# Kernel optimization log

Measured on AMD Instinct MI355X. Metric: run time of the kernel, lower is better.

Reference implementation:

```python
import jax, jax.numpy as jnp
import numpy as np

N, M, B = 1024, 8192, 8192  # W: [N, M], x: [B, N]
BLOCK = 32


def activation_quant(x):
    # per-tensor symmetric int8 fake-quant with STE
    scale = 127.0 / jnp.clip(jnp.max(jnp.abs(x)), 1e-8, None)
    x_q = jnp.clip(jnp.round(x * scale), -128.0, 127.0) / scale
    return x + jax.lax.stop_gradient(x_q - x)


def weight_quant_q2_k(w, block_size=BLOCK):
    # blockwise 2-bit quant with top-2 outliers kept at 4-bit, STE
    shape = w.shape
    wf = w.reshape(-1)
    n = wf.shape[0]
    pad = (-n) % block_size
    wf = jnp.pad(wf, (0, pad))
    blocks = wf.reshape(-1, block_size)
    scales = jnp.clip(jnp.max(jnp.abs(blocks), axis=1, keepdims=True), 1e-8, None)
    nb = blocks / scales
    k = min(2, block_size)
    _, top_idx = jax.lax.top_k(jnp.abs(nb), k)
    rows = jnp.arange(nb.shape[0])[:, None]
    top_mask = jnp.zeros(nb.shape, dtype=bool).at[rows, top_idx].set(True)
    q4 = jnp.round(nb * 7.0) / 7.0
    abs_nb = jnp.abs(nb)
    q2 = jnp.sign(nb) * jnp.where(abs_nb > 0.66, 1.0, 1.0 / 3.0)
    q = jnp.where(top_mask, q4, q2) * scales
    w_q = q.reshape(-1)[:n].reshape(shape)
    return w + jax.lax.stop_gradient(w_q - w)


def setup_inputs() -> dict:
    key = jax.random.key(0)
    k1, k2, k3 = jax.random.split(key, 3)
    x = jax.random.normal(k1, (B, N), dtype=jnp.float32)
    W = jax.random.normal(k2, (N, M), dtype=jnp.float32) / np.float32(np.sqrt(M))
    b = jax.random.normal(k3, (N,), dtype=jnp.float32)
    idx = jnp.arange(M // 2, dtype=jnp.int32)            # expanded (quantized) columns
    idx_comp = jnp.arange(M // 2, M, dtype=jnp.int32)    # continuous columns
    return {"x": x, "W": W, "b": b, "idx": idx, "idx_comp": idx_comp}


def reference(x, W, b, idx, idx_comp):
    W_exp_q = weight_quant_q2_k(jnp.take(W, idx, axis=1))   # [N, M/2]
    W_cont = jnp.take(W, idx_comp, axis=1)                  # [N, M/2]
    hidden_exp = activation_quant(x) @ W_exp_q              # [B, M/2]
    hidden_cont = x @ W_cont                                # [B, M/2]
    hidden = (jnp.zeros((x.shape[0], M), dtype=x.dtype)
              .at[:, idx].set(hidden_exp)
              .at[:, idx_comp].set(hidden_cont))            # scatter back to [B, M]
    h_exp = activation_quant(hidden[:, idx])
    out = jax.nn.relu(h_exp @ W_exp_q.T + hidden[:, idx_comp] @ W_cont.T + b)
    return out
```

## Files before the change

### kernel.cpp

```cpp
#include <hip/hip_runtime.h>
#include <hip/hip_bf16.h>
#include <cstdint>


using bf16x8 = __attribute__((ext_vector_type(8))) __bf16;
using f32x4  = __attribute__((ext_vector_type(4))) float;

typedef const __attribute__((address_space(1))) void g_void;
typedef __attribute__((address_space(3))) void l_void;

__device__ __forceinline__ void gload16(const void* g, void* l) {
  __builtin_amdgcn_global_load_lds((g_void*)g, (l_void*)l, 16, 0, 0);
}

__device__ __forceinline__ ushort f2bf(float f) {
  union { float f; unsigned u; } c; c.f = f;
  unsigned r = c.u + 0x7FFFu + ((c.u >> 16) & 1u);
  return (ushort)(r >> 16);
}
__device__ __forceinline__ float bf2f(ushort u) {
  union { unsigned u; float f; } c; c.u = ((unsigned)u) << 16;
  return c.f;
}

__global__ void prep_wa_kernel(const float* __restrict__ W,
                               const float4* __restrict__ x,
                               ushort* __restrict__ Wq,
                               ushort* __restrict__ WqT,
                               ushort* __restrict__ Wcb,
                               unsigned* __restrict__ amax_bits) {
  const int bidx = blockIdx.x;
  const int tid = threadIdx.x;

  if (bidx < 1024) {
    __shared__ __align__(16) ushort tile[64][72];
    const int rt = bidx >> 6;
    const int ct = bidx & 63;
    const int r0 = rt * 64, c0 = ct * 64;
    const int e = tid & 31;
    const int hw = tid >> 5;
    #pragma unroll
    for (int it = 0; it < 16; ++it) {
      const int g = it * 8 + hw;
      const int row = g >> 1;
      const int cg = (g & 1) * 32;
      const float w = W[(size_t)(r0 + row) * 8192 + c0 + cg + e];
      float aw = fabsf(w);
      float m = aw;
      #pragma unroll
      for (int d = 1; d <= 16; d <<= 1) m = fmaxf(m, __shfl_xor(m, d));
      int idx = (aw == m) ? e : 32;
      #pragma unroll
      for (int d = 1; d <= 16; d <<= 1) idx = min(idx, __shfl_xor(idx, d));
      const int i1 = idx;
      float a2 = (e == i1) ? -1.f : aw;
      float m2 = a2;
      #pragma unroll
      for (int d = 1; d <= 16; d <<= 1) m2 = fmaxf(m2, __shfl_xor(m2, d));
      int idx2 = (a2 == m2) ? e : 32;
      #pragma unroll
      for (int d = 1; d <= 16; d <<= 1) idx2 = min(idx2, __shfl_xor(idx2, d));
      const int i2 = idx2;

      const float scale = fmaxf(m, 1e-8f);
      const float nb = w / scale;
      float q;
      if (e == i1 || e == i2) {
        q = rintf(nb * 7.f) / 7.f;
      } else {
        float s = (nb > 0.f) ? 1.f : ((nb < 0.f) ? -1.f : 0.f);
        q = s * ((fabsf(nb) > 0.66f) ? 1.f : (1.f / 3.f));
      }
      const ushort qb = f2bf(q * scale);
      Wq[(size_t)(r0 + row) * 4096 + c0 + cg + e] = qb;
      tile[cg + e][row] = qb;
    }
    __syncthreads();
    const int c = tid >> 2;
    const int q4 = (tid & 3) * 16;
    uint4 v0 = *(const uint4*)&tile[c][q4];
    uint4 v1 = *(const uint4*)&tile[c][q4 + 8];
    *(uint4*)(WqT + (size_t)(c0 + c) * 1024 + r0 + q4) = v0;
    *(uint4*)(WqT + (size_t)(c0 + c) * 1024 + r0 + q4 + 8) = v1;
  } else if (bidx < 5120) {
    const int u = (bidx - 1024) * 256 + tid;
    const int row = u >> 10;
    const int c4 = u & 1023;
    float4 v = *(const float4*)(W + (size_t)row * 8192 + 4096 + c4 * 4);
    ushort4 o;
    o.x = f2bf(v.x); o.y = f2bf(v.y); o.z = f2bf(v.z); o.w = f2bf(v.w);
    *(ushort4*)(Wcb + (size_t)row * 4096 + c4 * 4) = o;
  } else {
    float m = 0.f;
    const int base = (bidx - 5120) * 256 + tid;
    const int stride = 2048 * 256;
    for (int i = base; i < 8192 * 1024 / 4; i += stride) {
      float4 v = x[i];
      m = fmaxf(m, fmaxf(fmaxf(fabsf(v.x), fabsf(v.y)),
                         fmaxf(fabsf(v.z), fabsf(v.w))));
    }
    #pragma unroll
    for (int off = 32; off > 0; off >>= 1) m = fmaxf(m, __shfl_down(m, off));
    __shared__ float wm[4];
    int lane = tid & 63, wave = tid >> 6;
    if (lane == 0) wm[wave] = m;
    __syncthreads();
    if (tid == 0) {
      float r = fmaxf(fmaxf(wm[0], wm[1]), fmaxf(wm[2], wm[3]));
      atomicMax(amax_bits, __float_as_uint(r));
    }
  }
}

__global__ void prep_x_kernel(const float4* __restrict__ x,
                              const unsigned* __restrict__ amax_bits,
                              uint4* __restrict__ xq, uint4* __restrict__ xbf) {
  const float amax = fmaxf(__uint_as_float(*amax_bits), 1e-8f);
  const float scale = 127.f / amax;
  const int base = blockIdx.x * 256 + threadIdx.x;
  const int stride = 2048 * 256;
  const int n8 = 8192 * 1024 / 8;
  for (int i = base; i < n8; i += stride) {
    float4 a = x[i * 2], b = x[i * 2 + 1];
    float v[8] = {a.x, a.y, a.z, a.w, b.x, b.y, b.z, b.w};
    unsigned qw[4], bw[4];
    #pragma unroll
    for (int j = 0; j < 4; ++j) {
      float q0 = fminf(fmaxf(rintf(v[2 * j] * scale), -128.f), 127.f) / scale;
      float q1 = fminf(fmaxf(rintf(v[2 * j + 1] * scale), -128.f), 127.f) / scale;
      qw[j] = (unsigned)f2bf(q0) | ((unsigned)f2bf(q1) << 16);
      bw[j] = (unsigned)f2bf(v[2 * j]) | ((unsigned)f2bf(v[2 * j + 1]) << 16);
    }
    xq[i] = make_uint4(qw[0], qw[1], qw[2], qw[3]);
    xbf[i] = make_uint4(bw[0], bw[1], bw[2], bw[3]);
  }
}

__global__ __launch_bounds__(256, 2) void gemm1_kernel(
    const ushort* __restrict__ Wcb,
    ushort* __restrict__ G,
    const ushort* __restrict__ Aq, const ushort* __restrict__ BT,
    ushort* __restrict__ Hexp, unsigned* __restrict__ amax_bits) {
  __shared__ __align__(16) ushort As[2][128 * 32];
  __shared__ __align__(16) ushort Bs[2][128 * 32];
  __shared__ float wredmax[4];

  const int bidx = blockIdx.x;
  const int tid = threadIdx.x;
  const int lane = tid & 63, wave = tid >> 6;
  const int l15 = lane & 15, quad = lane >> 4;
  const int wm = (wave >> 1) << 6, wn = (wave & 1) << 6;
  const int sel = (quad ^ ((l15 >> 1) & 3)) * 8;
  const int scs = ((tid & 3) ^ ((tid >> 3) & 3)) * 8;

  ushort* Asl0 = As[0] + tid * 8; ushort* Asl1 = As[1] + tid * 8;
  ushort* Bsl0 = Bs[0] + tid * 8; ushort* Bsl1 = Bs[1] + tid * 8;

  f32x4 acc[4][4];
  #pragma unroll
  for (int i = 0; i < 4; ++i)
    #pragma unroll
    for (int j = 0; j < 4; ++j) acc[i][j] = (f32x4){0.f, 0.f, 0.f, 0.f};

  if (bidx < 64) {
    const int gy = bidx >> 3, gx = bidx & 7;
    const int i0 = gy * 128, j0 = gx * 128;
    const ushort* Ag = Wcb + (size_t)(i0 + (tid >> 2)) * 4096 + scs;
    const ushort* Bg = Wcb + (size_t)(j0 + (tid >> 2)) * 4096 + scs;
    for (int k0 = 0; k0 < 4096; k0 += 64) {
      __syncthreads();
      gload16(Ag + k0, Asl0);
      gload16(Ag + (size_t)64 * 4096 + k0, Asl0 + 64 * 32);
      gload16(Bg + k0, Bsl0);
      gload16(Bg + (size_t)64 * 4096 + k0, Bsl0 + 64 * 32);
      gload16(Ag + k0 + 32, Asl1);
      gload16(Ag + (size_t)64 * 4096 + k0 + 32, Asl1 + 64 * 32);
      gload16(Bg + k0 + 32, Bsl1);
      gload16(Bg + (size_t)64 * 4096 + k0 + 32, Bsl1 + 64 * 32);
      __syncthreads();
      #pragma unroll
      for (int p = 0; p < 2; ++p) {
        bf16x8 af[4], bfr[4];
        #pragma unroll
        for (int i = 0; i < 4; ++i)
          af[i] = *(const bf16x8*)&As[p][(wm + i * 16 + l15) * 32 + sel];
        #pragma unroll
        for (int j = 0; j < 4; ++j)
          bfr[j] = *(const bf16x8*)&Bs[p][(wn + j * 16 + l15) * 32 + sel];
        #pragma unroll
        for (int i = 0; i < 4; ++i)
          #pragma unroll
          for (int j = 0; j < 4; ++j)
            acc[i][j] = __builtin_amdgcn_mfma_f32_16x16x32_bf16(af[i], bfr[j], acc[i][j], 0, 0, 0);
      }
    }
    const int row0 = i0 + wm + quad * 4;
    const int col0 = j0 + wn + l15;
    #pragma unroll
    for (int i = 0; i < 4; ++i)
      #pragma unroll
      for (int j = 0; j < 4; ++j)
        #pragma unroll
        for (int r = 0; r < 4; ++r)
          G[(size_t)(row0 + i * 16 + r) * 1024 + (col0 + j * 16)] = f2bf(acc[i][j][r]);
    return;
  }

  const int l = bidx - 64;
  const int xcd = l & 7;
  const int s = l >> 3;
  const int t = (xcd << 2) | (s >> 6);
  const int u = s & 63;
  const int bx = ((t & 3) << 3) | (u & 7);
  const int by = ((t >> 2) << 3) | (u >> 3);

  const ushort* Ag = Aq + (size_t)(by * 128 + (tid >> 2)) * 1024 + scs;
  const ushort* Bg = BT + (size_t)(bx * 128 + (tid >> 2)) * 1024 + scs;

  for (int k0 = 0; k0 < 1024; k0 += 64) {
    __syncthreads();
    gload16(Ag + k0, Asl0);
    gload16(Ag + 64 * 1024 + k0, Asl0 + 64 * 32);
    gload16(Bg + k0, Bsl0);
    gload16(Bg + 64 * 1024 + k0, Bsl0 + 64 * 32);
    gload16(Ag + k0 + 32, Asl1);
    gload16(Ag + 64 * 1024 + k0 + 32, Asl1 + 64 * 32);
    gload16(Bg + k0 + 32, Bsl1);
    gload16(Bg + 64 * 1024 + k0 + 32, Bsl1 + 64 * 32);
    __syncthreads();

    #pragma unroll
    for (int p = 0; p < 2; ++p) {
      bf16x8 af[4], bfr[4];
      #pragma unroll
      for (int i = 0; i < 4; ++i)
        af[i] = *(const bf16x8*)&As[p][(wm + i * 16 + l15) * 32 + sel];
      #pragma unroll
      for (int j = 0; j < 4; ++j)
        bfr[j] = *(const bf16x8*)&Bs[p][(wn + j * 16 + l15) * 32 + sel];
      #pragma unroll
      for (int i = 0; i < 4; ++i)
        #pragma unroll
        for (int j = 0; j < 4; ++j)
          acc[i][j] = __builtin_amdgcn_mfma_f32_16x16x32_bf16(af[i], bfr[j], acc[i][j], 0, 0, 0);
    }
  }

  const int row0 = by * 128 + wm + quad * 4;
  const int col0 = bx * 128 + wn + l15;
  float lmax = 0.f;
  #pragma unroll
  for (int i = 0; i < 4; ++i)
    #pragma unroll
    for (int j = 0; j < 4; ++j)
      #pragma unroll
      for (int r = 0; r < 4; ++r) {
        float v = acc[i][j][r];
        lmax = fmaxf(lmax, fabsf(v));
        Hexp[(size_t)(row0 + i * 16 + r) * 4096 + (col0 + j * 16)] = f2bf(v);
      }

  #pragma unroll
  for (int off = 32; off > 0; off >>= 1)
    lmax = fmaxf(lmax, __shfl_down(lmax, off));
  if (lane == 0) wredmax[wave] = lmax;
  __syncthreads();
  if (tid == 0) {
    float m = fmaxf(fmaxf(wredmax[0], wredmax[1]), fmaxf(wredmax[2], wredmax[3]));
    atomicMax(amax_bits, __float_as_uint(m));
  }
}

__global__ void quant_h_kernel(ushort* __restrict__ H,
                               const unsigned* __restrict__ amax_bits) {
  const float amax = fmaxf(__uint_as_float(*amax_bits), 1e-8f);
  const float scale = 127.f / amax;
  const int n8 = 8192 * 4096 / 8;
  for (int i = blockIdx.x * blockDim.x + threadIdx.x; i < n8;
       i += gridDim.x * blockDim.x) {
    uint4* p = (uint4*)H + i;
    uint4 a = *p;
    unsigned w[4] = {a.x, a.y, a.z, a.w};
    #pragma unroll
    for (int j = 0; j < 4; ++j) {
      float lo = bf2f((ushort)(w[j] & 0xFFFF));
      float hi = bf2f((ushort)(w[j] >> 16));
      lo = fminf(fmaxf(rintf(lo * scale), -128.f), 127.f) / scale;
      hi = fminf(fmaxf(rintf(hi * scale), -128.f), 127.f) / scale;
      w[j] = (unsigned)f2bf(lo) | ((unsigned)f2bf(hi) << 16);
    }
    *p = make_uint4(w[0], w[1], w[2], w[3]);
  }
}

__global__ __launch_bounds__(256, 2) void gemm2_kernel(
    const ushort* __restrict__ Hq, const ushort* __restrict__ Wq,
    const ushort* __restrict__ Xb, const ushort* __restrict__ G,
    const float* __restrict__ bias, float* __restrict__ out) {
  __shared__ __align__(16) ushort As[2][128 * 32];
  __shared__ __align__(16) ushort Bs[2][128 * 32];

  const int l = blockIdx.x;
  const int xcd = l & 7;
  const int s = l >> 3;
  const int by = (xcd << 3) | (s >> 3);
  const int bx = s & 7;

  const int tid = threadIdx.x;
  const int lane = tid & 63, wave = tid >> 6;
  const int wm = (wave >> 1) << 6, wn = (wave & 1) << 6;
  const int l15 = lane & 15, quad = lane >> 4;
  const int sel = (quad ^ ((l15 >> 1) & 3)) * 8;
  const int scs = ((tid & 3) ^ ((tid >> 3) & 3)) * 8;

  ushort* Asl0 = As[0] + tid * 8; ushort* Asl1 = As[1] + tid * 8;
  ushort* Bsl0 = Bs[0] + tid * 8; ushort* Bsl1 = Bs[1] + tid * 8;

  f32x4 acc[4][4];
  #pragma unroll
  for (int i = 0; i < 4; ++i)
    #pragma unroll
    for (int j = 0; j < 4; ++j) acc[i][j] = (f32x4){0.f, 0.f, 0.f, 0.f};

  {
    const ushort* Ag = Hq + (size_t)(by * 128 + (tid >> 2)) * 4096 + scs;
    const ushort* Bg = Wq + (size_t)(bx * 128 + (tid >> 2)) * 4096 + scs;
    for (int k0 = 0; k0 < 4096; k0 += 64) {
      __syncthreads();
      gload16(Ag + k0, Asl0);
      gload16(Ag + (size_t)64 * 4096 + k0, Asl0 + 64 * 32);
      gload16(Bg + k0, Bsl0);
      gload16(Bg + (size_t)64 * 4096 + k0, Bsl0 + 64 * 32);
      gload16(Ag + k0 + 32, Asl1);
      gload16(Ag + (size_t)64 * 4096 + k0 + 32, Asl1 + 64 * 32);
      gload16(Bg + k0 + 32, Bsl1);
      gload16(Bg + (size_t)64 * 4096 + k0 + 32, Bsl1 + 64 * 32);
      __syncthreads();
      #pragma unroll
      for (int p = 0; p < 2; ++p) {
        bf16x8 af[4], bfr[4];
        #pragma unroll
        for (int i = 0; i < 4; ++i)
          af[i] = *(const bf16x8*)&As[p][(wm + i * 16 + l15) * 32 + sel];
        #pragma unroll
        for (int j = 0; j < 4; ++j)
          bfr[j] = *(const bf16x8*)&Bs[p][(wn + j * 16 + l15) * 32 + sel];
        #pragma unroll
        for (int i = 0; i < 4; ++i)
          #pragma unroll
          for (int j = 0; j < 4; ++j)
            acc[i][j] = __builtin_amdgcn_mfma_f32_16x16x32_bf16(af[i], bfr[j], acc[i][j], 0, 0, 0);
      }
    }
  }
  {
    const ushort* Ag = Xb + (size_t)(by * 128 + (tid >> 2)) * 1024 + scs;
    const ushort* Bg = G + (size_t)(bx * 128 + (tid >> 2)) * 1024 + scs;
    for (int k0 = 0; k0 < 1024; k0 += 64) {
      __syncthreads();
      gload16(Ag + k0, Asl0);
      gload16(Ag + 64 * 1024 + k0, Asl0 + 64 * 32);
      gload16(Bg + k0, Bsl0);
      gload16(Bg + 64 * 1024 + k0, Bsl0 + 64 * 32);
      gload16(Ag + k0 + 32, Asl1);
      gload16(Ag + 64 * 1024 + k0 + 32, Asl1 + 64 * 32);
      gload16(Bg + k0 + 32, Bsl1);
      gload16(Bg + 64 * 1024 + k0 + 32, Bsl1 + 64 * 32);
      __syncthreads();
      #pragma unroll
      for (int p = 0; p < 2; ++p) {
        bf16x8 af[4], bfr[4];
        #pragma unroll
        for (int i = 0; i < 4; ++i)
          af[i] = *(const bf16x8*)&As[p][(wm + i * 16 + l15) * 32 + sel];
        #pragma unroll
        for (int j = 0; j < 4; ++j)
          bfr[j] = *(const bf16x8*)&Bs[p][(wn + j * 16 + l15) * 32 + sel];
        #pragma unroll
        for (int i = 0; i < 4; ++i)
          #pragma unroll
          for (int j = 0; j < 4; ++j)
            acc[i][j] = __builtin_amdgcn_mfma_f32_16x16x32_bf16(af[i], bfr[j], acc[i][j], 0, 0, 0);
      }
    }
  }

  const int row0 = by * 128 + wm + quad * 4;
  const int col0 = bx * 128 + wn + l15;
  #pragma unroll
  for (int i = 0; i < 4; ++i)
    #pragma unroll
    for (int j = 0; j < 4; ++j) {
      float bv = bias[col0 + j * 16];
      #pragma unroll
      for (int r = 0; r < 4; ++r) {
        float v = acc[i][j][r] + bv;
        v = fmaxf(v, 0.f);
        out[(size_t)(row0 + i * 16 + r) * 1024 + (col0 + j * 16)] = v;
      }
    }
}

extern "C" void kernel_launch(void* const* d_in, const int* in_sizes, int n_in,
                              void* d_out, int out_size, void* d_ws, size_t ws_size,
                              hipStream_t stream) {
  (void)in_sizes; (void)n_in; (void)out_size; (void)ws_size;
  const float* x = (const float*)d_in[0];
  const float* W = (const float*)d_in[1];
  const float* b = (const float*)d_in[2];

  char* ws = (char*)d_ws;
  unsigned* scal = (unsigned*)ws;
  ushort* xq   = (ushort*)(ws + 256);
  ushort* xbf  = xq   + (size_t)8192 * 1024;
  ushort* Wq   = xbf  + (size_t)8192 * 1024;
  ushort* WqT  = Wq   + (size_t)1024 * 4096;
  ushort* Wcb  = WqT  + (size_t)4096 * 1024;
  ushort* G    = Wcb  + (size_t)1024 * 4096;
  ushort* Hexp = G    + (size_t)1024 * 1024;

  hipMemsetAsync(scal, 0, 256, stream);
  prep_wa_kernel<<<7168, 256, 0, stream>>>(W, (const float4*)x, Wq, WqT, Wcb, scal);
  prep_x_kernel<<<2048, 256, 0, stream>>>((const float4*)x, scal,
                                          (uint4*)xq, (uint4*)xbf);
  gemm1_kernel<<<2112, 256, 0, stream>>>(Wcb, G, xq, WqT, Hexp, scal + 1);
  quant_h_kernel<<<4096, 256, 0, stream>>>(Hexp, scal + 1);
  gemm2_kernel<<<512, 256, 0, stream>>>(Hexp, Wq, xbf, G, b, (float*)d_out);
}
```

Measured before the change: 341.5 us.

## Fuse prep and quant stages into persistent kernels with grid barriers

Merges prep_wa and prep_x into one persistent 512-block kernel that uses a software grid barrier after the x amax reduction. gemm1 and the H quantisation are merged the same way: each block handles several output tiles, joins a grid barrier on the global amax, then re-quantises its own tiles while they are likely still in cache. This removes two kernel launches and one full standalone pass over H. In exchange it relies on all 512 blocks being co-resident to avoid deadlock, and the persistent grid may load-balance the tiles less evenly.

```diff
diff --git a/kernel.cpp b/kernel.cpp
--- a/kernel.cpp
+++ b/kernel.cpp
@@ -23,22 +23,74 @@
   return c.f;
 }
 
-__global__ void prep_wa_kernel(const float* __restrict__ W,
-                               const float4* __restrict__ x,
-                               ushort* __restrict__ Wq,
-                               ushort* __restrict__ WqT,
-                               ushort* __restrict__ Wcb,
-                               unsigned* __restrict__ amax_bits) {
-  const int bidx = blockIdx.x;
+__device__ __forceinline__ void gridbar(unsigned* cnt) {
+  __syncthreads();
+  if (threadIdx.x == 0) {
+    __threadfence();
+    __hip_atomic_fetch_add(cnt, 1u, __ATOMIC_ACQ_REL, __HIP_MEMORY_SCOPE_AGENT);
+    while (__hip_atomic_load(cnt, __ATOMIC_ACQUIRE, __HIP_MEMORY_SCOPE_AGENT) <
+           512u)
+      __builtin_amdgcn_s_sleep(2);
+  }
+  __syncthreads();
+}
+
+template <int STRIDE>
+__device__ __forceinline__ void kloop(const ushort* Ag, const ushort* Bg,
+                                      int kbeg, int kend, ushort* As, ushort* Bs,
+                                      f32x4 (&acc)[4][4], int wm, int wn,
+                                      int l15, int quad, int sel) {
   const int tid = threadIdx.x;
-
-  if (bidx < 1024) {
-    __shared__ __align__(16) ushort tile[64][72];
-    const int rt = bidx >> 6;
-    const int ct = bidx & 63;
+  ushort* Asl0 = As + tid * 8;        ushort* Asl1 = As + 4096 + tid * 8;
+  ushort* Bsl0 = Bs + tid * 8;        ushort* Bsl1 = Bs + 4096 + tid * 8;
+  for (int k0 = kbeg; k0 < kend; k0 += 64) {
+    __syncthreads();
+    gload16(Ag + k0, Asl0);
+    gload16(Ag + (size_t)64 * STRIDE + k0, Asl0 + 64 * 32);
+    gload16(Bg + k0, Bsl0);
+    gload16(Bg + (size_t)64 * STRIDE + k0, Bsl0 + 64 * 32);
+    gload16(Ag + k0 + 32, Asl1);
+    gload16(Ag + (size_t)64 * STRIDE + k0 + 32, Asl1 + 64 * 32);
+    gload16(Bg + k0 + 32, Bsl1);
+    gload16(Bg + (size_t)64 * STRIDE + k0 + 32, Bsl1 + 64 * 32);
+    __syncthreads();
+    #pragma unroll
+    for (int p = 0; p < 2; ++p) {
+      bf16x8 af[4], bfr[4];
+      #pragma unroll
+      for (int i = 0; i < 4; ++i)
+        af[i] = *(const bf16x8*)&As[p * 4096 + (wm + i * 16 + l15) * 32 + sel];
+      #pragma unroll
+      for (int j = 0; j < 4; ++j)
+        bfr[j] = *(const bf16x8*)&Bs[p * 4096 + (wn + j * 16 + l15) * 32 + sel];
+      #pragma unroll
+      for (int i = 0; i < 4; ++i)
+        #pragma unroll
+        for (int j = 0; j < 4; ++j)
+          acc[i][j] = __builtin_amdgcn_mfma_f32_16x16x32_bf16(af[i], bfr[j],
+                                                              acc[i][j], 0, 0, 0);
+    }
+  }
+}
+
+__global__ __launch_bounds__(256, 2) void prep_kernel(
+    const float* __restrict__ W, const float4* __restrict__ x,
+    ushort* __restrict__ Wq, ushort* __restrict__ WqT,
+    ushort* __restrict__ Wcb, unsigned* __restrict__ bar,
+    unsigned* __restrict__ amaxx,
+    uint4* __restrict__ xq, uint4* __restrict__ xbf) {
+  __shared__ __align__(16) ushort tile[64][72];
+  __shared__ float sred[4];
+  const int b = blockIdx.x;
+  const int tid = threadIdx.x;
+  const int lane = tid & 63, wave = tid >> 6;
+
+  #pragma unroll 1
+  for (int tt = 0; tt < 2; ++tt) {
+    const int t = b * 2 + tt;
+    const int rt = t >> 6, ct = t & 63;
     const int r0 = rt * 64, c0 = ct * 64;
-    const int e = tid & 31;
-    const int hw = tid >> 5;
+    const int e = tid & 31, hw = tid >> 5;
     #pragma unroll
     for (int it = 0; it < 16; ++it) {
       const int g = it * 8 + hw;
@@ -82,47 +134,44 @@
     uint4 v1 = *(const uint4*)&tile[c][q4 + 8];
     *(uint4*)(WqT + (size_t)(c0 + c) * 1024 + r0 + q4) = v0;
     *(uint4*)(WqT + (size_t)(c0 + c) * 1024 + r0 + q4 + 8) = v1;
-  } else if (bidx < 5120) {
-    const int u = (bidx - 1024) * 256 + tid;
+    __syncthreads();
+  }
+
+  for (int u = b * 256 + tid; u < 1024 * 1024; u += 512 * 256) {
     const int row = u >> 10;
     const int c4 = u & 1023;
     float4 v = *(const float4*)(W + (size_t)row * 8192 + 4096 + c4 * 4);
     ushort4 o;
     o.x = f2bf(v.x); o.y = f2bf(v.y); o.z = f2bf(v.z); o.w = f2bf(v.w);
     *(ushort4*)(Wcb + (size_t)row * 4096 + c4 * 4) = o;
-  } else {
+  }
+
+  {
     float m = 0.f;
-    const int base = (bidx - 5120) * 256 + tid;
-    const int stride = 2048 * 256;
-    for (int i = base; i < 8192 * 1024 / 4; i += stride) {
+    for (int i = b * 256 + tid; i < 8192 * 1024 / 4; i += 512 * 256) {
       float4 v = x[i];
       m = fmaxf(m, fmaxf(fmaxf(fabsf(v.x), fabsf(v.y)),
                          fmaxf(fabsf(v.z), fabsf(v.w))));
     }
     #pragma unroll
     for (int off = 32; off > 0; off >>= 1) m = fmaxf(m, __shfl_down(m, off));
-    __shared__ float wm[4];
-    int lane = tid & 63, wave = tid >> 6;
-    if (lane == 0) wm[wave] = m;
+    if (lane == 0) sred[wave] = m;
     __syncthreads();
     if (tid == 0) {
-      float r = fmaxf(fmaxf(wm[0], wm[1]), fmaxf(wm[2], wm[3]));
-      atomicMax(amax_bits, __float_as_uint(r));
-    }
-  }
-}
-
-__global__ void prep_x_kernel(const float4* __restrict__ x,
-                              const unsigned* __restrict__ amax_bits,
-                              uint4* __restrict__ xq, uint4* __restrict__ xbf) {
-  const float amax = fmaxf(__uint_as_float(*amax_bits), 1e-8f);
+      float r = fmaxf(fmaxf(sred[0], sred[1]), fmaxf(sred[2], sred[3]));
+      atomicMax(amaxx, __float_as_uint(r));
+    }
+  }
+  gridbar(&bar[0]);
+
+  const float amax = fmaxf(
+      __uint_as_float(__hip_atomic_load(amaxx, __ATOMIC_ACQUIRE,
+                                        __HIP_MEMORY_SCOPE_AGENT)),
+      1e-8f);
   const float scale = 127.f / amax;
-  const int base = blockIdx.x * 256 + threadIdx.x;
-  const int stride = 2048 * 256;
-  const int n8 = 8192 * 1024 / 8;
-  for (int i = base; i < n8; i += stride) {
-    float4 a = x[i * 2], b = x[i * 2 + 1];
-    float v[8] = {a.x, a.y, a.z, a.w, b.x, b.y, b.z, b.w};
+  for (int i = b * 256 + tid; i < 8192 * 1024 / 8; i += 512 * 256) {
+    float4 a = x[i * 2], v2 = x[i * 2 + 1];
+    float v[8] = {a.x, a.y, a.z, a.w, v2.x, v2.y, v2.z, v2.w};
     unsigned qw[4], bw[4];
     #pragma unroll
     for (int j = 0; j < 4; ++j) {
@@ -137,15 +186,14 @@
 }
 
 __global__ __launch_bounds__(256, 2) void gemm1_kernel(
-    const ushort* __restrict__ Wcb,
-    ushort* __restrict__ G,
+    const ushort* __restrict__ Wcb, ushort* __restrict__ G,
     const ushort* __restrict__ Aq, const ushort* __restrict__ BT,
-    ushort* __restrict__ Hexp, unsigned* __restrict__ amax_bits) {
-  __shared__ __align__(16) ushort As[2][128 * 32];
-  __shared__ __align__(16) ushort Bs[2][128 * 32];
-  __shared__ float wredmax[4];
-
-  const int bidx = blockIdx.x;
+    ushort* __restrict__ Hexp, unsigned* __restrict__ bar,
+    unsigned* __restrict__ amaxh) {
+  __shared__ __align__(16) ushort As[8192];
+  __shared__ __align__(16) ushort Bs[8192];
+  __shared__ float sred[4];
+  const int b = blockIdx.x;
   const int tid = threadIdx.x;
   const int lane = tid & 63, wave = tid >> 6;
   const int l15 = lane & 15, quad = lane >> 4;
@@ -153,47 +201,17 @@
   const int sel = (quad ^ ((l15 >> 1) & 3)) * 8;
   const int scs = ((tid & 3) ^ ((tid >> 3) & 3)) * 8;
 
-  ushort* Asl0 = As[0] + tid * 8; ushort* Asl1 = As[1] + tid * 8;
-  ushort* Bsl0 = Bs[0] + tid * 8; ushort* Bsl1 = Bs[1] + tid * 8;
-
-  f32x4 acc[4][4];
-  #pragma unroll
-  for (int i = 0; i < 4; ++i)
-    #pragma unroll
-    for (int j = 0; j < 4; ++j) acc[i][j] = (f32x4){0.f, 0.f, 0.f, 0.f};
-
-  if (bidx < 64) {
-    const int gy = bidx >> 3, gx = bidx & 7;
+  if (b < 64) {
+    const int gy = b >> 3, gx = b & 7;
     const int i0 = gy * 128, j0 = gx * 128;
+    f32x4 acc[4][4];
+    #pragma unroll
+    for (int i = 0; i < 4; ++i)
+      #pragma unroll
+      for (int j = 0; j < 4; ++j) acc[i][j] = (f32x4){0.f, 0.f, 0.f, 0.f};
     const ushort* Ag = Wcb + (size_t)(i0 + (tid >> 2)) * 4096 + scs;
     const ushort* Bg = Wcb + (size_t)(j0 + (tid >> 2)) * 4096 + scs;
-    for (int k0 = 0; k0 < 4096; k0 += 64) {
-      __syncthreads();
-      gload16(Ag + k0, Asl0);
-      gload16(Ag + (size_t)64 * 4096 + k0, Asl0 + 64 * 32);
-      gload16(Bg + k0, Bsl0);
-      gload16(Bg + (size_t)64 * 4096 + k0, Bsl0 + 64 * 32);
-      gload16(Ag + k0 + 32, Asl1);
-      gload16(Ag + (size_t)64 * 4096 + k0 + 32, Asl1 + 64 * 32);
-      gload16(Bg + k0 + 32, Bsl1);
-      gload16(Bg + (size_t)64 * 4096 + k0 + 32, Bsl1 + 64 * 32);
-      __syncthreads();
-      #pragma unroll
-      for (int p = 0; p < 2; ++p) {
-        bf16x8 af[4], bfr[4];
-        #pragma unroll
-        for (int i = 0; i < 4; ++i)
-          af[i] = *(const bf16x8*)&As[p][(wm + i * 16 + l15) * 32 + sel];
-        #pragma unroll
-        for (int j = 0; j < 4; ++j)
-          bfr[j] = *(const bf16x8*)&Bs[p][(wn + j * 16 + l15) * 32 + sel];
-        #pragma unroll
-        for (int i = 0; i < 4; ++i)
-          #pragma unroll
-          for (int j = 0; j < 4; ++j)
-            acc[i][j] = __builtin_amdgcn_mfma_f32_16x16x32_bf16(af[i], bfr[j], acc[i][j], 0, 0, 0);
-      }
-    }
+    kloop<4096>(Ag, Bg, 0, 4096, As, Bs, acc, wm, wn, l15, quad, sel);
     const int row0 = i0 + wm + quad * 4;
     const int col0 = j0 + wn + l15;
     #pragma unroll
@@ -202,94 +220,86 @@
       for (int j = 0; j < 4; ++j)
         #pragma unroll
         for (int r = 0; r < 4; ++r)
-          G[(size_t)(row0 + i * 16 + r) * 1024 + (col0 + j * 16)] = f2bf(acc[i][j][r]);
+          G[(size_t)(row0 + i * 16 + r) * 1024 + (col0 + j * 16)] =
+              f2bf(acc[i][j][r]);
+    gridbar(&bar[1]);
     return;
   }
 
-  const int l = bidx - 64;
-  const int xcd = l & 7;
-  const int s = l >> 3;
-  const int t = (xcd << 2) | (s >> 6);
-  const int u = s & 63;
-  const int bx = ((t & 3) << 3) | (u & 7);
-  const int by = ((t >> 2) << 3) | (u >> 3);
-
-  const ushort* Ag = Aq + (size_t)(by * 128 + (tid >> 2)) * 1024 + scs;
-  const ushort* Bg = BT + (size_t)(bx * 128 + (tid >> 2)) * 1024 + scs;
-
-  for (int k0 = 0; k0 < 1024; k0 += 64) {
-    __syncthreads();
-    gload16(Ag + k0, Asl0);
-    gload16(Ag + 64 * 1024 + k0, Asl0 + 64 * 32);
-    gload16(Bg + k0, Bsl0);
-    gload16(Bg + 64 * 1024 + k0, Bsl0 + 64 * 32);
-    gload16(Ag + k0 + 32, Asl1);
-    gload16(Ag + 64 * 1024 + k0 + 32, Asl1 + 64 * 32);
-    gload16(Bg + k0 + 32, Bsl1);
-    gload16(Bg + 64 * 1024 + k0 + 32, Bsl1 + 64 * 32);
-    __syncthreads();
-
-    #pragma unroll
-    for (int p = 0; p < 2; ++p) {
-      bf16x8 af[4], bfr[4];
-      #pragma unroll
-      for (int i = 0; i < 4; ++i)
-        af[i] = *(const bf16x8*)&As[p][(wm + i * 16 + l15) * 32 + sel];
+  const int iB = b - 64;
+  const int ntiles = (iB < 256) ? 5 : 4;
+  float lmax = 0.f;
+  #pragma unroll 1
+  for (int k = 0; k < ntiles; ++k) {
+    const int t = iB + k * 448;
+    const int xcd = t & 7;
+    const int s = t >> 3;
+    const int tt = (xcd << 2) | (s >> 6);
+    const int uu = s & 63;
+    const int bx = ((tt & 3) << 3) | (uu & 7);
+    const int by = ((tt >> 2) << 3) | (uu >> 3);
+    f32x4 acc[4][4];
+    #pragma unroll
+    for (int i = 0; i < 4; ++i)
+      #pragma unroll
+      for (int j = 0; j < 4; ++j) acc[i][j] = (f32x4){0.f, 0.f, 0.f, 0.f};
+    const ushort* Ag = Aq + (size_t)(by * 128 + (tid >> 2)) * 1024 + scs;
+    const ushort* Bg = BT + (size_t)(bx * 128 + (tid >> 2)) * 1024 + scs;
+    kloop<1024>(Ag, Bg, 0, 1024, As, Bs, acc, wm, wn, l15, quad, sel);
+    const int row0 = by * 128 + wm + quad * 4;
+    const int col0 = bx * 128 + wn + l15;
+    #pragma unroll
+    for (int i = 0; i < 4; ++i)
       #pragma unroll
       for (int j = 0; j < 4; ++j)
-        bfr[j] = *(const bf16x8*)&Bs[p][(wn + j * 16 + l15) * 32 + sel];
-      #pragma unroll
-      for (int i = 0; i < 4; ++i)
         #pragma unroll
-        for (int j = 0; j < 4; ++j)
-          acc[i][j] = __builtin_amdgcn_mfma_f32_16x16x32_bf16(af[i], bfr[j], acc[i][j], 0, 0, 0);
-    }
-  }
-
-  const int row0 = by * 128 + wm + quad * 4;
-  const int col0 = bx * 128 + wn + l15;
-  float lmax = 0.f;
-  #pragma unroll
-  for (int i = 0; i < 4; ++i)
-    #pragma unroll
-    for (int j = 0; j < 4; ++j)
-      #pragma unroll
-      for (int r = 0; r < 4; ++r) {
-        float v = acc[i][j][r];
-        lmax = fmaxf(lmax, fabsf(v));
-        Hexp[(size_t)(row0 + i * 16 + r) * 4096 + (col0 + j * 16)] = f2bf(v);
-      }
-
+        for (int r = 0; r < 4; ++r) {
+          float v = acc[i][j][r];
+          lmax = fmaxf(lmax, fabsf(v));
+          Hexp[(size_t)(row0 + i * 16 + r) * 4096 + (col0 + j * 16)] = f2bf(v);
+        }
+  }
   #pragma unroll
   for (int off = 32; off > 0; off >>= 1)
     lmax = fmaxf(lmax, __shfl_down(lmax, off));
-  if (lane == 0) wredmax[wave] = lmax;
+  if (lane == 0) sred[wave] = lmax;
   __syncthreads();
   if (tid == 0) {
-    float m = fmaxf(fmaxf(wredmax[0], wredmax[1]), fmaxf(wredmax[2], wredmax[3]));
-    atomicMax(amax_bits, __float_as_uint(m));
-  }
-}
-
-__global__ void quant_h_kernel(ushort* __restrict__ H,
-                               const unsigned* __restrict__ amax_bits) {
-  const float amax = fmaxf(__uint_as_float(*amax_bits), 1e-8f);
+    float m = fmaxf(fmaxf(sred[0], sred[1]), fmaxf(sred[2], sred[3]));
+    atomicMax(amaxh, __float_as_uint(m));
+  }
+  gridbar(&bar[1]);
+
+  const float amax = fmaxf(
+      __uint_as_float(__hip_atomic_load(amaxh, __ATOMIC_ACQUIRE,
+                                        __HIP_MEMORY_SCOPE_AGENT)),
+      1e-8f);
   const float scale = 127.f / amax;
-  const int n8 = 8192 * 4096 / 8;
-  for (int i = blockIdx.x * blockDim.x + threadIdx.x; i < n8;
-       i += gridDim.x * blockDim.x) {
-    uint4* p = (uint4*)H + i;
-    uint4 a = *p;
-    unsigned w[4] = {a.x, a.y, a.z, a.w};
-    #pragma unroll
-    for (int j = 0; j < 4; ++j) {
-      float lo = bf2f((ushort)(w[j] & 0xFFFF));
-      float hi = bf2f((ushort)(w[j] >> 16));
-      lo = fminf(fmaxf(rintf(lo * scale), -128.f), 127.f) / scale;
-      hi = fminf(fmaxf(rintf(hi * scale), -128.f), 127.f) / scale;
-      w[j] = (unsigned)f2bf(lo) | ((unsigned)f2bf(hi) << 16);
-    }
-    *p = make_uint4(w[0], w[1], w[2], w[3]);
+  #pragma unroll 1
+  for (int k = 0; k < ntiles; ++k) {
+    const int t = iB + k * 448;
+    const int xcd = t & 7;
+    const int s = t >> 3;
+    const int tt = (xcd << 2) | (s >> 6);
+    const int uu = s & 63;
+    const int bx = ((tt & 3) << 3) | (uu & 7);
+    const int by = ((tt >> 2) << 3) | (uu >> 3);
+    for (int q = tid; q < 2048; q += 256) {
+      const int row = q >> 4, c16 = q & 15;
+      uint4* p = (uint4*)(Hexp + (size_t)(by * 128 + row) * 4096 + bx * 128 +
+                          c16 * 8);
+      uint4 a = *p;
+      unsigned w[4] = {a.x, a.y, a.z, a.w};
+      #pragma unroll
+      for (int j = 0; j < 4; ++j) {
+        float lo = bf2f((ushort)(w[j] & 0xFFFF));
+        float hi = bf2f((ushort)(w[j] >> 16));
+        lo = fminf(fmaxf(rintf(lo * scale), -128.f), 127.f) / scale;
+        hi = fminf(fmaxf(rintf(hi * scale), -128.f), 127.f) / scale;
+        w[j] = (unsigned)f2bf(lo) | ((unsigned)f2bf(hi) << 16);
+      }
+      *p = make_uint4(w[0], w[1], w[2], w[3]);
+    }
   }
 }
 
@@ -297,8 +307,8 @@
     const ushort* __restrict__ Hq, const ushort* __restrict__ Wq,
     const ushort* __restrict__ Xb, const ushort* __restrict__ G,
     const float* __restrict__ bias, float* __restrict__ out) {
-  __shared__ __align__(16) ushort As[2][128 * 32];
-  __shared__ __align__(16) ushort Bs[2][128 * 32];
+  __shared__ __align__(16) ushort As[8192];
+  __shared__ __align__(16) ushort Bs[8192];
 
   const int l = blockIdx.x;
   const int xcd = l & 7;
@@ -313,9 +323,6 @@
   const int sel = (quad ^ ((l15 >> 1) & 3)) * 8;
   const int scs = ((tid & 3) ^ ((tid >> 3) & 3)) * 8;
 
-  ushort* Asl0 = As[0] + tid * 8; ushort* Asl1 = As[1] + tid * 8;
-  ushort* Bsl0 = Bs[0] + tid * 8; ushort* Bsl1 = Bs[1] + tid * 8;
-
   f32x4 acc[4][4];
   #pragma unroll
   for (int i = 0; i < 4; ++i)
@@ -325,64 +332,12 @@
   {
     const ushort* Ag = Hq + (size_t)(by * 128 + (tid >> 2)) * 4096 + scs;
     const ushort* Bg = Wq + (size_t)(bx * 128 + (tid >> 2)) * 4096 + scs;
-    for (int k0 = 0; k0 < 4096; k0 += 64) {
-      __syncthreads();
-      gload16(Ag + k0, Asl0);
-      gload16(Ag + (size_t)64 * 4096 + k0, Asl0 + 64 * 32);
-      gload16(Bg + k0, Bsl0);
-      gload16(Bg + (size_t)64 * 4096 + k0, Bsl0 + 64 * 32);
-      gload16(Ag + k0 + 32, Asl1);
-      gload16(Ag + (size_t)64 * 4096 + k0 + 32, Asl1 + 64 * 32);
-      gload16(Bg + k0 + 32, Bsl1);
-      gload16(Bg + (size_t)64 * 4096 + k0 + 32, Bsl1 + 64 * 32);
-      __syncthreads();
-      #pragma unroll
-      for (int p = 0; p < 2; ++p) {
-        bf16x8 af[4], bfr[4];
-        #pragma unroll
-        for (int i = 0; i < 4; ++i)
-          af[i] = *(const bf16x8*)&As[p][(wm + i * 16 + l15) * 32 + sel];
-        #pragma unroll
-        for (int j = 0; j < 4; ++j)
-          bfr[j] = *(const bf16x8*)&Bs[p][(wn + j * 16 + l15) * 32 + sel];
-        #pragma unroll
-        for (int i = 0; i < 4; ++i)
-          #pragma unroll
-          for (int j = 0; j < 4; ++j)
-            acc[i][j] = __builtin_amdgcn_mfma_f32_16x16x32_bf16(af[i], bfr[j], acc[i][j], 0, 0, 0);
-      }
-    }
+    kloop<4096>(Ag, Bg, 0, 4096, As, Bs, acc, wm, wn, l15, quad, sel);
   }
   {
     const ushort* Ag = Xb + (size_t)(by * 128 + (tid >> 2)) * 1024 + scs;
     const ushort* Bg = G + (size_t)(bx * 128 + (tid >> 2)) * 1024 + scs;
-    for (int k0 = 0; k0 < 1024; k0 += 64) {
-      __syncthreads();
-      gload16(Ag + k0, Asl0);
-      gload16(Ag + 64 * 1024 + k0, Asl0 + 64 * 32);
-      gload16(Bg + k0, Bsl0);
-      gload16(Bg + 64 * 1024 + k0, Bsl0 + 64 * 32);
-      gload16(Ag + k0 + 32, Asl1);
-      gload16(Ag + 64 * 1024 + k0 + 32, Asl1 + 64 * 32);
-      gload16(Bg + k0 + 32, Bsl1);
-      gload16(Bg + 64 * 1024 + k0 + 32, Bsl1 + 64 * 32);
-      __syncthreads();
-      #pragma unroll
-      for (int p = 0; p < 2; ++p) {
-        bf16x8 af[4], bfr[4];
-        #pragma unroll
-        for (int i = 0; i < 4; ++i)
-          af[i] = *(const bf16x8*)&As[p][(wm + i * 16 + l15) * 32 + sel];
-        #pragma unroll
-        for (int j = 0; j < 4; ++j)
-          bfr[j] = *(const bf16x8*)&Bs[p][(wn + j * 16 + l15) * 32 + sel];
-        #pragma unroll
-        for (int i = 0; i < 4; ++i)
-          #pragma unroll
-          for (int j = 0; j < 4; ++j)
-            acc[i][j] = __builtin_amdgcn_mfma_f32_16x16x32_bf16(af[i], bfr[j], acc[i][j], 0, 0, 0);
-      }
-    }
+    kloop<1024>(Ag, Bg, 0, 1024, As, Bs, acc, wm, wn, l15, quad, sel);
   }
 
   const int row0 = by * 128 + wm + quad * 4;
@@ -410,8 +365,10 @@
   const float* b = (const float*)d_in[2];
 
   char* ws = (char*)d_ws;
-  unsigned* scal = (unsigned*)ws;
-  ushort* xq   = (ushort*)(ws + 256);
+  unsigned* bar   = (unsigned*)ws;
+  unsigned* amaxh = (unsigned*)(ws + 64);
+  unsigned* amaxx = (unsigned*)(ws + 72);
+  ushort* xq   = (ushort*)(ws + 16384);
   ushort* xbf  = xq   + (size_t)8192 * 1024;
   ushort* Wq   = xbf  + (size_t)8192 * 1024;
   ushort* WqT  = Wq   + (size_t)1024 * 4096;
@@ -419,11 +376,9 @@
   ushort* G    = Wcb  + (size_t)1024 * 4096;
   ushort* Hexp = G    + (size_t)1024 * 1024;
 
-  hipMemsetAsync(scal, 0, 256, stream);
-  prep_wa_kernel<<<7168, 256, 0, stream>>>(W, (const float4*)x, Wq, WqT, Wcb, scal);
-  prep_x_kernel<<<2048, 256, 0, stream>>>((const float4*)x, scal,
-                                          (uint4*)xq, (uint4*)xbf);
-  gemm1_kernel<<<2112, 256, 0, stream>>>(Wcb, G, xq, WqT, Hexp, scal + 1);
-  quant_h_kernel<<<4096, 256, 0, stream>>>(Hexp, scal + 1);
+  hipMemsetAsync(ws, 0, 128, stream);
+  prep_kernel<<<512, 256, 0, stream>>>(W, (const float4*)x, Wq, WqT, Wcb, bar,
+                                       amaxx, (uint4*)xq, (uint4*)xbf);
+  gemm1_kernel<<<512, 256, 0, stream>>>(Wcb, G, xq, WqT, Hexp, bar, amaxh);
   gemm2_kernel<<<512, 256, 0, stream>>>(Hexp, Wq, xbf, G, b, (float*)d_out);
 }
```

Result: slower. 600.3 us (+75.8%).
